# Kernel tuning notes

Hardware: AMD Instinct MI355X
Metric: run time of the kernel (lower is better)

The kernel has to match this reference:

```python
import jax, jax.numpy as jnp
import numpy as np

N_NODES = 50000
N_EDGES = 640000
D = 128
L = 3


def setup_inputs() -> dict:
    key = jax.random.key(0)
    k1, k2, k3, k4 = jax.random.split(key, 4)
    x = jax.random.normal(k1, (N_NODES, D), dtype=jnp.float32)
    # Glorot-ish scale so activations stay O(1) across 3 layers
    Ws = jax.random.normal(k2, (L, D, D), dtype=jnp.float32) * (1.0 / np.sqrt(D))
    bs = jnp.zeros((L, D), dtype=jnp.float32)
    edge_src = jax.random.randint(k3, (N_EDGES,), 0, N_NODES, dtype=jnp.int32)
    edge_dst = jax.random.randint(k4, (N_EDGES,), 0, N_NODES, dtype=jnp.int32)
    return {"x": x, "Ws": Ws, "bs": bs, "edge_src": edge_src, "edge_dst": edge_dst}


def reference(x, Ws, bs, edge_src, edge_dst):
    n = x.shape[0]
    ones = jnp.ones(edge_src.shape[0], dtype=x.dtype)
    # degrees, clamped to 1 as in dgl GraphConv(norm='both')
    deg_out = jnp.maximum(jax.ops.segment_sum(ones, edge_src, num_segments=n), 1.0)
    deg_in = jnp.maximum(jax.ops.segment_sum(ones, edge_dst, num_segments=n), 1.0)
    inv_sqrt_out = jax.lax.rsqrt(deg_out)[:, None]  # [N,1]
    inv_sqrt_in = jax.lax.rsqrt(deg_in)[:, None]    # [N,1]
    for l in range(Ws.shape[0]):
        h = x * inv_sqrt_out                         # src normalization
        msg = h[edge_src]                            # [E,D] gather
        agg = jax.ops.segment_sum(msg, edge_dst, num_segments=n)  # [N,D] scatter-add
        h = agg * inv_sqrt_in                        # dst normalization
        x = jax.nn.relu(h @ Ws[l] + bs[l])           # linear + ReLU
    return x
```

## Files before the change

### kernel.cpp

```cpp
#include <hip/hip_runtime.h>
#include <hip/hip_fp16.h>

typedef __attribute__((ext_vector_type(8))) _Float16 half8;
typedef __attribute__((ext_vector_type(4))) float f32x4;
typedef unsigned int u32;
typedef unsigned short u16;
typedef unsigned long long u64;

#define ELL_PAD 64
#define BKT 128
#define BKT_SH 7
#define EPB 2048
#define NAMAX 512
#define RUNCAP 3072


__global__ __launch_bounds__(256) void initpack(int* __restrict__ deg_out,
                                                u32* __restrict__ xz0,
                                                u32* __restrict__ xz1,
                                                const float* __restrict__ Ws,
                                                _Float16* __restrict__ Whi,
                                                _Float16* __restrict__ Wlo,
                                                int N, int padU32, int zb, int packTotal) {
  int b = blockIdx.x;
  if (b < zb) {
    int i = b * 256 + threadIdx.x;
    if (i < N) deg_out[i] = 0;
    if (b == 0) {
      for (int j = threadIdx.x; j < padU32; j += 256) { xz0[j] = 0; xz1[j] = 0; }
    }
    return;
  }
  int i = (b - zb) * 256 + threadIdx.x;
  if (i < packTotal) {
    int lane  = i & 63;
    int kstep = (i >> 6) & 3;
    int ntile = (i >> 8) & 7;
    int layer = i >> 11;
    int nn = ntile * 16 + (lane & 15);
    int k0 = kstep * 32 + (lane >> 4) * 8;
    const float* W = Ws + (size_t)layer * 128 * 128;
    size_t base = (size_t)i * 8;
    for (int j = 0; j < 8; j++) {
      float v = W[(k0 + j) * 128 + nn];
      _Float16 hi = (_Float16)v;
      Whi[base + j] = hi;
      Wlo[base + j] = (_Float16)(v - (float)hi);
    }
  }
}


__global__ __launch_bounds__(512) void parta(const int* __restrict__ esrc,
                                             const int* __restrict__ edst,
                                             int* __restrict__ deg_out,
                                             u32* __restrict__ part,
                                             u32* __restrict__ runTab,
                                             int E, int NB) {
  __shared__ u32 hist[512];
  __shared__ u32 stage[EPB];
  __shared__ u32 scanA[512];
  int a = blockIdx.x;
  int e0 = a * EPB;
  int e1 = min(E, e0 + EPB);
  int len = e1 - e0;
  int tid = threadIdx.x;
  if (tid <= NB) hist[tid] = 0;
  __syncthreads();
  for (int i = e0 + tid; i < e1; i += 512) {
    int s = esrc[i];
    int d = edst[i];
    atomicAdd(&deg_out[s], 1);
    atomicAdd(&hist[d >> BKT_SH], 1u);
  }
  __syncthreads();
  u32 myc = (tid < NB) ? hist[tid] : 0;
  scanA[tid] = myc;
  __syncthreads();
  for (int off = 1; off < NB; off <<= 1) {
    u32 t = scanA[tid] + ((tid >= off) ? scanA[tid - off] : 0);
    __syncthreads();
    scanA[tid] = t;
    __syncthreads();
  }
  u32 excl = scanA[tid] - myc;
  u32* rt = runTab + (size_t)a * (NB + 1);
  if (tid < NB) { rt[tid] = excl; hist[tid] = excl; }
  if (tid == 0) rt[NB] = (u32)len;
  __syncthreads();
  for (int i = e0 + tid; i < e1; i += 512) {
    int s = esrc[i];
    int d = edst[i];
    u32 p = atomicAdd(&hist[d >> BKT_SH], 1u);
    stage[p] = (u32)s | ((u32)(d & (BKT - 1)) << 16);
  }
  __syncthreads();
  u32* op = part + (size_t)a * EPB;
  for (int j = tid; j < len; j += 512) op[j] = stage[j];
}


__global__ __launch_bounds__(512) void partb(const u32* __restrict__ part,
                                             const u32* __restrict__ runTab,
                                             const float* __restrict__ x,
                                             const int* __restrict__ deg_out,
                                             int* __restrict__ deg_in,
                                             u16* __restrict__ ell,
                                             __half2* __restrict__ xh,
                                             int N, int NA, int NB) {
  __shared__ u16 slice[BKT * ELL_PAD];
  __shared__ u32 cnt2[BKT * 17];
  __shared__ u32 roff[NAMAX + 1];
  __shared__ u32 rbase[NAMAX];
  __shared__ u16 runid[RUNCAP];
  __shared__ u32 pstage[RUNCAP];
  __shared__ u32 scanA[512];
  int b = blockIdx.x;
  int base = b * BKT;
  int hi = min(BKT, N - base);
  if (hi <= 0) return;
  int tid = threadIdx.x;

  u32 nv = ((u32)N << 16) | (u32)N;
  u32* s32 = (u32*)slice;
  for (int j = tid; j < BKT * (ELL_PAD / 2); j += 512) s32[j] = nv;
  for (int j = tid; j < BKT * 17; j += 512) cnt2[j] = 0;
  u32 mylen = 0;
  if (tid < NA) {
    u32 s = runTab[(size_t)tid * (NB + 1) + b];
    u32 e = runTab[(size_t)tid * (NB + 1) + b + 1];
    mylen = e - s;
    rbase[tid] = (u32)tid * EPB + s;
  }
  scanA[tid] = mylen;
  __syncthreads();
  for (int off = 1; off < NA + 1; off <<= 1) {
    u32 t = scanA[tid] + ((tid >= off) ? scanA[tid - off] : 0);
    __syncthreads();
    scanA[tid] = t;
    __syncthreads();
  }
  if (tid <= NA) roff[tid] = scanA[tid] - mylen;
  __syncthreads();
  int T = (int)roff[NA];
  for (int a = tid; a < NA; a += 512) {
    u32 s0 = roff[a];
    u32 l  = roff[a + 1] - s0;
    for (u32 k = 0; k < l; k++)
      if (s0 + k < RUNCAP) runid[s0 + k] = (u16)a;
  }
  __syncthreads();
  for (int i = tid; i < T; i += 512) {
    int a;
    if (i < RUNCAP) a = runid[i];
    else {
      int lo = 0, hh = NA;
      while (hh - lo > 1) { int mid = (lo + hh) >> 1; if (roff[mid] <= (u32)i) lo = mid; else hh = mid; }
      a = lo;
    }
    u32 pair = part[(size_t)rbase[a] + ((u32)i - roff[a])];
    if (i < RUNCAP) pstage[i] = pair;
    u32 dl  = pair >> 16;
    u32 src = pair & 0xFFFFu;
    atomicAdd(&cnt2[dl * 17 + (src >> 12)], 1u);
  }
  __syncthreads();
  if (tid < BKT) {
    u32 run = 0;
    for (int bk = 0; bk < 16; bk++) {
      u32 t = cnt2[tid * 17 + bk];
      cnt2[tid * 17 + bk] = run;
      run += t;
    }
    if (tid < hi) deg_in[base + tid] = (int)run;
  }
  __syncthreads();
  for (int i = tid; i < T; i += 512) {
    u32 pair;
    if (i < RUNCAP) pair = pstage[i];
    else {
      int lo = 0, hh = NA;
      while (hh - lo > 1) { int mid = (lo + hh) >> 1; if (roff[mid] <= (u32)i) lo = mid; else hh = mid; }
      pair = part[(size_t)rbase[lo] + ((u32)i - roff[lo])];
    }
    u32 dl  = pair >> 16;
    u32 src = pair & 0xFFFFu;
    u32 p = atomicAdd(&cnt2[dl * 17 + (src >> 12)], 1u);
    if (p < ELL_PAD) slice[dl * ELL_PAD + p] = (u16)src;
  }
  __syncthreads();
  u32* eg = (u32*)(ell + (size_t)base * ELL_PAD);
  for (int j = tid; j < hi * (ELL_PAD / 2); j += 512) eg[j] = s32[j];
  float* sc = (float*)scanA;
  if (tid < hi) {
    int d = deg_out[base + tid]; if (d < 1) d = 1;
    sc[tid] = rsqrtf((float)d);
  }
  __syncthreads();
  for (int j = tid; j < hi * 64; j += 512) {
    int r = j >> 6, c = j & 63;
    float s = sc[r];
    float2 v = ((const float2*)x)[(size_t)(base + r) * 64 + c];
    xh[(size_t)(base + r) * 64 + c] = __floats2half2_rn(v.x * s, v.y * s);
  }
}


__global__ __launch_bounds__(256) void gath8(const _Float16* __restrict__ xh,
                                             const int* __restrict__ deg_in,
                                             const u16* __restrict__ ell,
                                             _Float16* __restrict__ agg, int n) {
  const int wave = (int)threadIdx.x >> 6;
  const int lane = (int)threadIdx.x & 63;
  const int sub  = lane & 15;
  const int grp  = lane >> 4;
  const int sh   = grp << 4;
  const u32 sub16 = (u32)sub * 16u;
  const char* __restrict__ xb = (const char*)xh;

  int r0 = blockIdx.x * 8 + wave * 2, r1 = r0 + 1;
  int d0 = (r0 < n) ? deg_in[r0] : 0;
  int d1 = (r1 < n) ? deg_in[r1] : 0;
  int l0 = d0 > ELL_PAD ? ELL_PAD : d0;
  int l1 = d1 > ELL_PAD ? ELL_PAD : d1;
  int t0 = (l0 + 3) & ~3;
  int t1 = (l1 + 3) & ~3;
  const u16* ep0 = ell + (u32)(r0 < n ? r0 : 0) * ELL_PAD;
  const u16* ep1 = ell + (u32)(r1 < n ? r1 : 0) * ELL_PAD;

  float a0[8] = {0.f, 0.f, 0.f, 0.f, 0.f, 0.f, 0.f, 0.f};
  float a1[8] = {0.f, 0.f, 0.f, 0.f, 0.f, 0.f, 0.f, 0.f};

  int m = t0 < t1 ? t0 : t1;
  int e = 0;
  for (; e + 8 <= m; e += 8) {
    u64 wa0 = *(const u64*)&ep0[e];
    u64 wa1 = *(const u64*)&ep0[e + 4];
    u64 wb0 = *(const u64*)&ep1[e];
    u64 wb1 = *(const u64*)&ep1[e + 4];
    u32 ia0 = ((u32)(wa0 >> sh) & 0xFFFFu) * 256u + sub16;
    u32 ia1 = ((u32)(wa1 >> sh) & 0xFFFFu) * 256u + sub16;
    u32 ib0 = ((u32)(wb0 >> sh) & 0xFFFFu) * 256u + sub16;
    u32 ib1 = ((u32)(wb1 >> sh) & 0xFFFFu) * 256u + sub16;
    half8 va0 = *(const half8*)(xb + ia0);
    half8 va1 = *(const half8*)(xb + ia1);
    half8 vb0 = *(const half8*)(xb + ib0);
    half8 vb1 = *(const half8*)(xb + ib1);
#pragma unroll
    for (int j = 0; j < 8; j++) {
      a0[j] += (float)va0[j] + (float)va1[j];
      a1[j] += (float)vb0[j] + (float)vb1[j];
    }
  }
  for (; e < m; e += 4) {
    u64 wa = *(const u64*)&ep0[e];
    u64 wb = *(const u64*)&ep1[e];
    u32 ia = ((u32)(wa >> sh) & 0xFFFFu) * 256u + sub16;
    u32 ib = ((u32)(wb >> sh) & 0xFFFFu) * 256u + sub16;
    half8 va = *(const half8*)(xb + ia);
    half8 vb = *(const half8*)(xb + ib);
#pragma unroll
    for (int j = 0; j < 8; j++) { a0[j] += (float)va[j]; a1[j] += (float)vb[j]; }
  }
  for (int ea = m; ea < t0; ea += 4) {
    u64 wa = *(const u64*)&ep0[ea];
    u32 ia = ((u32)(wa >> sh) & 0xFFFFu) * 256u + sub16;
    half8 va = *(const half8*)(xb + ia);
#pragma unroll
    for (int j = 0; j < 8; j++) a0[j] += (float)va[j];
  }
  for (int eb = m; eb < t1; eb += 4) {
    u64 wb = *(const u64*)&ep1[eb];
    u32 ib = ((u32)(wb >> sh) & 0xFFFFu) * 256u + sub16;
    half8 vb = *(const half8*)(xb + ib);
#pragma unroll
    for (int j = 0; j < 8; j++) a1[j] += (float)vb[j];
  }

#pragma unroll
  for (int j = 0; j < 8; j++) {
    a0[j] += __shfl_xor(a0[j], 16, 64);
    a0[j] += __shfl_xor(a0[j], 32, 64);
    a1[j] += __shfl_xor(a1[j], 16, 64);
    a1[j] += __shfl_xor(a1[j], 32, 64);
  }

  float si0 = rsqrtf((float)(d0 < 1 ? 1 : d0));
  float si1 = rsqrtf((float)(d1 < 1 ? 1 : d1));
  if (grp == 0) {
    half8 h0, h1;
#pragma unroll
    for (int j = 0; j < 8; j++) {
      h0[j] = (_Float16)(a0[j] * si0);
      h1[j] = (_Float16)(a1[j] * si1);
    }
    *(half8*)&agg[(size_t)r0 * 128 + sub * 8] = h0;
    *(half8*)&agg[(size_t)r1 * 128 + sub * 8] = h1;
  }
}


__global__ __launch_bounds__(512) void mm64(const _Float16* __restrict__ agg,
                                            const _Float16* __restrict__ Whi,
                                            const _Float16* __restrict__ Wlo,
                                            const float* __restrict__ bias,
                                            const int* __restrict__ deg_out,
                                            __half* __restrict__ out16,
                                            float* __restrict__ out32, int n) {
  __shared__ _Float16 As[64 * 136];
  const int wave = (int)threadIdx.x >> 6;
  const int lane = (int)threadIdx.x & 63;
  const int sub  = lane & 15;
  const int grp  = lane >> 4;
  const int rowBase = blockIdx.x * 64;

  for (int j = threadIdx.x; j < 64 * 16; j += 512) {
    int r = j >> 4, c = j & 15;
    *(half8*)&As[r * 136 + c * 8] =
        *(const half8*)&agg[(size_t)(rowBase + r) * 128 + c * 8];
  }
  half8 wh[4], wl[4];
#pragma unroll
  for (int ks = 0; ks < 4; ks++) {
    wh[ks] = *(const half8*)&Whi[((wave * 4 + ks) * 64 + lane) * 8];
    wl[ks] = *(const half8*)&Wlo[((wave * 4 + ks) * 64 + lane) * 8];
  }
  __syncthreads();

  const int col = wave * 16 + sub;
  const float bv = bias[col];
#pragma unroll
  for (int rt = 0; rt < 4; rt++) {
    f32x4 acc = (f32x4){0.f, 0.f, 0.f, 0.f};
#pragma unroll
    for (int ks = 0; ks < 4; ks++) {
      half8 a = *(const half8*)&As[(rt * 16 + sub) * 136 + ks * 32 + grp * 8];
      acc = __builtin_amdgcn_mfma_f32_16x16x32_f16(a, wh[ks], acc, 0, 0, 0);
      acc = __builtin_amdgcn_mfma_f32_16x16x32_f16(a, wl[ks], acc, 0, 0, 0);
    }
    int r0c = rowBase + rt * 16 + grp * 4;
#pragma unroll
    for (int r = 0; r < 4; r++) {
      int row = r0c + r;
      if (row < n) {
        float v = fmaxf(acc[r] + bv, 0.f);
        if (out16) {
          int d = deg_out[row]; if (d < 1) d = 1;
          out16[(size_t)row * 128 + col] = __float2half(v * rsqrtf((float)d));
        } else {
          out32[(size_t)row * 128 + col] = v;
        }
      }
    }
  }
}


extern "C" void kernel_launch(void* const* d_in, const int* in_sizes, int n_in,
                              void* d_out, int out_size, void* d_ws, size_t ws_size,
                              hipStream_t stream) {
  const float* x   = (const float*)d_in[0];
  const float* Ws  = (const float*)d_in[1];
  const float* bs  = (const float*)d_in[2];
  const int* esrc  = (const int*)d_in[3];
  const int* edst  = (const int*)d_in[4];

  const int D = 128;
  const int N = in_sizes[0] / D;
  const int E = in_sizes[3];
  const int L = in_sizes[1] / (D * D);
  const int Npad = ((N + 63) / 64) * 64;
  const int NA = (E + EPB - 1) / EPB;
  const int NB = (N + BKT - 1) / BKT;

  char* base = (char*)d_ws;
  size_t off = 0;
  auto alloc = [&](size_t bytes) {
    char* p = base + off;
    off = (off + bytes + 255) & ~(size_t)255;
    return p;
  };
  int*      deg_out = (int*)alloc((size_t)N * 4);
  int*      deg_in  = (int*)alloc((size_t)N * 4);
  u16*      ell     = (u16*)alloc((size_t)N * ELL_PAD * 2);
  _Float16* Whi     = (_Float16*)alloc((size_t)L * 16384 * 2);
  _Float16* Wlo     = (_Float16*)alloc((size_t)L * 16384 * 2);
  _Float16* xh0     = (_Float16*)alloc((size_t)(Npad + 16) * 128 * 2);
  _Float16* xh1     = (_Float16*)alloc((size_t)(Npad + 16) * 128 * 2);
  _Float16* agg     = (_Float16*)alloc((size_t)Npad * 128 * 2);
  u32*      part    = (u32*)alloc((size_t)NA * EPB * 4);
  u32*      runTab  = (u32*)alloc((size_t)NA * (NB + 1) * 4);

  const int zb = (N + 255) / 256;
  const int packTotal = L * 2048;
  const int packB = (packTotal + 255) / 256;
  const int padU32 = 16 * 64;

  initpack<<<dim3(zb + packB), dim3(256), 0, stream>>>(
      deg_out,
      (u32*)(xh0 + (size_t)N * 128), (u32*)(xh1 + (size_t)N * 128),
      Ws, Whi, Wlo, N, padU32, zb, packTotal);
  parta<<<dim3(NA), dim3(512), 0, stream>>>(
      esrc, edst, deg_out, part, runTab, E, NB);
  partb<<<dim3(NB), dim3(512), 0, stream>>>(
      part, runTab, x, deg_out, deg_in, ell, (__half2*)xh0, N, NA, NB);

  float* outf = (float*)d_out;
  _Float16* ping[2] = {xh0, xh1};

  for (int l = 0; l < L; l++) {
    bool last = (l == L - 1);
    gath8<<<dim3(Npad / 8), dim3(256), 0, stream>>>(
        (const _Float16*)ping[l & 1], deg_in, ell, agg, N);
    mm64<<<dim3(Npad / 64), dim3(512), 0, stream>>>(
        agg, Whi + (size_t)l * 16384, Wlo + (size_t)l * 16384,
        bs + (size_t)l * D, deg_out,
        last ? nullptr : (__half*)ping[(l + 1) & 1],
        last ? outf : nullptr, N);
  }
}
```

Before: 243.8 us.

## Split gather kernel across four feature-column quarters via grid y dimension

The gather kernel now launches four blocks per row group, each handling a 32-column quarter of the feature vector with 4-byte half2 loads instead of 16-byte half8 loads. This cuts per-thread accumulator registers and raises the number of blocks, aiming for more occupancy and memory-level parallelism on the random gathers. The cost is that the ELL index list and degrees are read four times, and each gather now moves smaller transactions, which may lower effective bandwidth per request.

After: 306.6 us. +25.8%, slower.

```diff
diff --git a/kernel.cpp b/kernel.cpp
--- a/kernel.cpp
+++ b/kernel.cpp
@@ -206,7 +206,7 @@
 }
 
 
-__global__ __launch_bounds__(256) void gath8(const _Float16* __restrict__ xh,
+__global__ __launch_bounds__(256) void gathq(const _Float16* __restrict__ xh,
                                              const int* __restrict__ deg_in,
                                              const u16* __restrict__ ell,
                                              _Float16* __restrict__ agg, int n) {
@@ -215,7 +215,8 @@
   const int sub  = lane & 15;
   const int grp  = lane >> 4;
   const int sh   = grp << 4;
-  const u32 sub16 = (u32)sub * 16u;
+  const int q    = blockIdx.y;
+  const u32 sub4 = (u32)q * 64u + (u32)sub * 4u;
   const char* __restrict__ xb = (const char*)xh;
 
   int r0 = blockIdx.x * 8 + wave * 2, r1 = r0 + 1;
@@ -228,8 +229,7 @@
   const u16* ep0 = ell + (u32)(r0 < n ? r0 : 0) * ELL_PAD;
   const u16* ep1 = ell + (u32)(r1 < n ? r1 : 0) * ELL_PAD;
 
-  float a0[8] = {0.f, 0.f, 0.f, 0.f, 0.f, 0.f, 0.f, 0.f};
-  float a1[8] = {0.f, 0.f, 0.f, 0.f, 0.f, 0.f, 0.f, 0.f};
+  float a0x = 0.f, a0y = 0.f, a1x = 0.f, a1y = 0.f;
 
   int m = t0 < t1 ? t0 : t1;
   int e = 0;
@@ -238,64 +238,52 @@
     u64 wa1 = *(const u64*)&ep0[e + 4];
     u64 wb0 = *(const u64*)&ep1[e];
     u64 wb1 = *(const u64*)&ep1[e + 4];
-    u32 ia0 = ((u32)(wa0 >> sh) & 0xFFFFu) * 256u + sub16;
-    u32 ia1 = ((u32)(wa1 >> sh) & 0xFFFFu) * 256u + sub16;
-    u32 ib0 = ((u32)(wb0 >> sh) & 0xFFFFu) * 256u + sub16;
-    u32 ib1 = ((u32)(wb1 >> sh) & 0xFFFFu) * 256u + sub16;
-    half8 va0 = *(const half8*)(xb + ia0);
-    half8 va1 = *(const half8*)(xb + ia1);
-    half8 vb0 = *(const half8*)(xb + ib0);
-    half8 vb1 = *(const half8*)(xb + ib1);
-#pragma unroll
-    for (int j = 0; j < 8; j++) {
-      a0[j] += (float)va0[j] + (float)va1[j];
-      a1[j] += (float)vb0[j] + (float)vb1[j];
-    }
+    u32 ia0 = ((u32)(wa0 >> sh) & 0xFFFFu) * 256u + sub4;
+    u32 ia1 = ((u32)(wa1 >> sh) & 0xFFFFu) * 256u + sub4;
+    u32 ib0 = ((u32)(wb0 >> sh) & 0xFFFFu) * 256u + sub4;
+    u32 ib1 = ((u32)(wb1 >> sh) & 0xFFFFu) * 256u + sub4;
+    float2 va0 = __half22float2(*(const __half2*)(xb + ia0));
+    float2 va1 = __half22float2(*(const __half2*)(xb + ia1));
+    float2 vb0 = __half22float2(*(const __half2*)(xb + ib0));
+    float2 vb1 = __half22float2(*(const __half2*)(xb + ib1));
+    a0x += va0.x + va1.x; a0y += va0.y + va1.y;
+    a1x += vb0.x + vb1.x; a1y += vb0.y + vb1.y;
   }
   for (; e < m; e += 4) {
     u64 wa = *(const u64*)&ep0[e];
     u64 wb = *(const u64*)&ep1[e];
-    u32 ia = ((u32)(wa >> sh) & 0xFFFFu) * 256u + sub16;
-    u32 ib = ((u32)(wb >> sh) & 0xFFFFu) * 256u + sub16;
-    half8 va = *(const half8*)(xb + ia);
-    half8 vb = *(const half8*)(xb + ib);
-#pragma unroll
-    for (int j = 0; j < 8; j++) { a0[j] += (float)va[j]; a1[j] += (float)vb[j]; }
+    u32 ia = ((u32)(wa >> sh) & 0xFFFFu) * 256u + sub4;
+    u32 ib = ((u32)(wb >> sh) & 0xFFFFu) * 256u + sub4;
+    float2 va = __half22float2(*(const __half2*)(xb + ia));
+    float2 vb = __half22float2(*(const __half2*)(xb + ib));
+    a0x += va.x; a0y += va.y;
+    a1x += vb.x; a1y += vb.y;
   }
   for (int ea = m; ea < t0; ea += 4) {
     u64 wa = *(const u64*)&ep0[ea];
-    u32 ia = ((u32)(wa >> sh) & 0xFFFFu) * 256u + sub16;
-    half8 va = *(const half8*)(xb + ia);
-#pragma unroll
-    for (int j = 0; j < 8; j++) a0[j] += (float)va[j];
+    u32 ia = ((u32)(wa >> sh) & 0xFFFFu) * 256u + sub4;
+    float2 va = __half22float2(*(const __half2*)(xb + ia));
+    a0x += va.x; a0y += va.y;
   }
   for (int eb = m; eb < t1; eb += 4) {
     u64 wb = *(const u64*)&ep1[eb];
-    u32 ib = ((u32)(wb >> sh) & 0xFFFFu) * 256u + sub16;
-    half8 vb = *(const half8*)(xb + ib);
-#pragma unroll
-    for (int j = 0; j < 8; j++) a1[j] += (float)vb[j];
-  }
-
-#pragma unroll
-  for (int j = 0; j < 8; j++) {
-    a0[j] += __shfl_xor(a0[j], 16, 64);
-    a0[j] += __shfl_xor(a0[j], 32, 64);
-    a1[j] += __shfl_xor(a1[j], 16, 64);
-    a1[j] += __shfl_xor(a1[j], 32, 64);
-  }
+    u32 ib = ((u32)(wb >> sh) & 0xFFFFu) * 256u + sub4;
+    float2 vb = __half22float2(*(const __half2*)(xb + ib));
+    a1x += vb.x; a1y += vb.y;
+  }
+
+  a0x += __shfl_xor(a0x, 16, 64); a0x += __shfl_xor(a0x, 32, 64);
+  a0y += __shfl_xor(a0y, 16, 64); a0y += __shfl_xor(a0y, 32, 64);
+  a1x += __shfl_xor(a1x, 16, 64); a1x += __shfl_xor(a1x, 32, 64);
+  a1y += __shfl_xor(a1y, 16, 64); a1y += __shfl_xor(a1y, 32, 64);
 
   float si0 = rsqrtf((float)(d0 < 1 ? 1 : d0));
   float si1 = rsqrtf((float)(d1 < 1 ? 1 : d1));
   if (grp == 0) {
-    half8 h0, h1;
-#pragma unroll
-    for (int j = 0; j < 8; j++) {
-      h0[j] = (_Float16)(a0[j] * si0);
-      h1[j] = (_Float16)(a1[j] * si1);
-    }
-    *(half8*)&agg[(size_t)r0 * 128 + sub * 8] = h0;
-    *(half8*)&agg[(size_t)r1 * 128 + sub * 8] = h1;
+    *(__half2*)&agg[(size_t)r0 * 128 + q * 32 + sub * 2] =
+        __floats2half2_rn(a0x * si0, a0y * si0);
+    *(__half2*)&agg[(size_t)r1 * 128 + q * 32 + sub * 2] =
+        __floats2half2_rn(a1x * si1, a1y * si1);
   }
 }
 
@@ -410,7 +398,7 @@
 
   for (int l = 0; l < L; l++) {
     bool last = (l == L - 1);
-    gath8<<<dim3(Npad / 8), dim3(256), 0, stream>>>(
+    gathq<<<dim3(Npad / 8, 4), dim3(256), 0, stream>>>(
         (const _Float16*)ping[l & 1], deg_in, ell, agg, N);
     mm64<<<dim3(Npad / 64), dim3(512), 0, stream>>>(
         agg, Whi + (size_t)l * 16384, Wlo + (size_t)l * 16384,
```
